# Kernel tuning notes

Measured on AMD Instinct MI355X. Metric: run time of the kernel, lower is better.

Reference implementation:

```python
import jax, jax.numpy as jnp
import numpy as np

C = 256
N_HEAD = 4
GROUPS = 32
EPS = 1e-5
B, H, W = 2, 64, 64


def group_norm(x, gamma, beta):
    # x: [B, C, H, W]; GroupNorm over (C//G, H, W) within each group
    b, c, h, w = x.shape
    xr = x.reshape(b, GROUPS, c // GROUPS, h, w)
    m = xr.mean(axis=(2, 3, 4), keepdims=True)
    v = xr.var(axis=(2, 3, 4), keepdims=True)
    xn = ((xr - m) * jax.lax.rsqrt(v + EPS)).reshape(b, c, h, w)
    return xn * gamma[None, :, None, None] + beta[None, :, None, None]


def setup_inputs() -> dict:
    key = jax.random.key(0)
    ks = jax.random.split(key, 5)
    s = 1.0 / np.sqrt(C)  # fan-in init scale for 1x1 convs
    return {
        "input": jax.random.normal(ks[0], (B, C, H, W), jnp.float32),
        "c": jax.random.normal(ks[1], (B, C, H, W), jnp.float32),
        "gn_w": jnp.ones((C,), jnp.float32),
        "gn_b": jnp.zeros((C,), jnp.float32),
        "wq": jax.random.normal(ks[2], (C, C), jnp.float32) * s,
        "wkv": jax.random.normal(ks[3], (2 * C, C), jnp.float32) * s,
        "wout_w": jax.random.normal(ks[4], (C, C), jnp.float32) * s,
        "wout_b": jnp.zeros((C,), jnp.float32),
    }


def reference(input, c, gn_w, gn_b, wq, wkv, wout_w, wout_b):
    b, ch, h, w = input.shape
    hd = ch // N_HEAD
    n = h * w
    # shared GroupNorm applied to both query source and context
    nq = group_norm(input, gn_w, gn_b)
    nkv = group_norm(c, gn_w, gn_b)
    # 1x1 convs == channel matmuls
    q = jnp.einsum('oc,bchw->bohw', wq, nq).reshape(b, N_HEAD, hd, n)
    kv = jnp.einsum('oc,bchw->bohw', wkv, nkv).reshape(b, N_HEAD, 2 * hd, n)
    k, v = jnp.split(kv, 2, axis=2)  # each [b, nh, hd, n]
    # NOTE: scale is 1/sqrt(channel), as in the source (not 1/sqrt(head_dim))
    attn = jnp.einsum('bncq,bnck->bnqk', q, k) / jnp.sqrt(jnp.float32(ch))
    attn = jax.nn.softmax(attn, axis=-1)
    o = jnp.einsum('bnqk,bnck->bncq', attn, v).reshape(b, ch, h, w)
    o = jnp.einsum('oc,bchw->bohw', wout_w, o) + wout_b[None, :, None, None]
    return o + input
```

## Files before the change

### kernel.cpp

```cpp
#include <hip/hip_runtime.h>


typedef __attribute__((ext_vector_type(8))) short short8;
typedef __attribute__((ext_vector_type(4))) short s4;
typedef __attribute__((ext_vector_type(4))) float f32x4;
typedef __attribute__((ext_vector_type(2))) unsigned int uint2v;

#if __has_builtin(__builtin_amdgcn_exp2f)
#define EXP2(x) __builtin_amdgcn_exp2f(x)
#else
#define EXP2(x) exp2f(x)
#endif

__device__ __forceinline__ unsigned short f2bf(float x) {
    unsigned int u = __builtin_bit_cast(unsigned int, x);
    u += 0x7FFFu + ((u >> 16) & 1u);
    return (unsigned short)(u >> 16);
}

__device__ __forceinline__ unsigned int pk2(float a, float b) {
    unsigned int ua = __builtin_bit_cast(unsigned int, a) + 0x8000u;
    unsigned int ub = __builtin_bit_cast(unsigned int, b) + 0x8000u;
    return (ua >> 16) | (ub & 0xFFFF0000u);
}

__device__ __forceinline__ short8 ld8(const unsigned short* p) {
    return *reinterpret_cast<const short8*>(p);
}

#define MFMA(a, b, c) __builtin_amdgcn_mfma_f32_16x16x32_bf16((a), (b), (c), 0, 0, 0)
#define MFMA16(a, b, c) __builtin_amdgcn_mfma_f32_16x16x16bf16_1k((a), (b), (c), 0, 0, 0)

__global__ __launch_bounds__(256) void gn_stats(const float* __restrict__ x0,
                                                const float* __restrict__ x1,
                                                float* __restrict__ statw) {
    int blk = blockIdx.x;
    int combo = blk >> 2, chunk = blk & 3;
    const float* x = (combo & 64) ? x1 : x0;
    int b = (combo >> 5) & 1, g = combo & 31;
    const float4* base = (const float4*)(x + (size_t)(b * 256 + g * 8) * 4096) + chunk * 2048;
    int tid = threadIdx.x, lane = tid & 63, w = tid >> 6;
    float s = 0.f, s2 = 0.f;
    for (int i = tid; i < 2048; i += 256) {
        float4 v = base[i];
        s  += v.x + v.y + v.z + v.w;
        s2 += v.x * v.x + v.y * v.y + v.z * v.z + v.w * v.w;
    }
    #pragma unroll
    for (int off = 32; off; off >>= 1) {
        s  += __shfl_down(s, off);
        s2 += __shfl_down(s2, off);
    }
    __shared__ float red[8];
    if (lane == 0) { red[w] = s; red[4 + w] = s2; }
    __syncthreads();
    if (tid == 0) {
        float* o = statw + (size_t)(combo * 4 + chunk) * 2;
        o[0] = red[0] + red[1] + red[2] + red[3];
        o[1] = red[4] + red[5] + red[6] + red[7];
    }
}

__global__ __launch_bounds__(256) void gn_norm(const float* __restrict__ x0,
                                               const float* __restrict__ x1,
                                               unsigned short* __restrict__ d0,
                                               unsigned short* __restrict__ d1,
                                               const float* __restrict__ statw,
                                               const float* __restrict__ gamma,
                                               const float* __restrict__ beta) {
    __shared__ unsigned short Xl[64 * 272];
    __shared__ float aL[256], bL[256];
    int blk = blockIdx.x;
    int t = blk >> 7, b = (blk >> 6) & 1, n0 = (blk & 63) * 64;
    const float* x = t ? x1 : x0;
    unsigned short* dst = t ? d1 : d0;
    int tid = threadIdx.x;
    {
        int c = tid, g = c >> 3;
        int combo = (t << 6) | (b << 5) | g;
        const float* sw = statw + (size_t)combo * 8;
        float S  = (sw[0] + sw[2]) + (sw[4] + sw[6]);
        float S2 = (sw[1] + sw[3]) + (sw[5] + sw[7]);
        float mean = S * (1.f / 32768.f);
        float var = S2 * (1.f / 32768.f) - mean * mean;
        float inv = rsqrtf(var + 1e-5f);
        float gm = gamma[c];
        aL[c] = gm * inv;
        bL[c] = beta[c] - mean * gm * inv;
    }
    __syncthreads();
    const float* xb = x + (size_t)b * 256 * 4096 + n0;
    #pragma unroll
    for (int it = 0; it < 16; it++) {
        int c = it * 16 + (tid >> 4);
        int n4 = tid & 15;
        float4 v = *(const float4*)(xb + (size_t)c * 4096 + n4 * 4);
        float a = aL[c], c0 = bL[c];
        int cs = c ^ ((n4 & 7) << 3);
        Xl[(n4 * 4 + 0) * 272 + cs] = f2bf(v.x * a + c0);
        Xl[(n4 * 4 + 1) * 272 + cs] = f2bf(v.y * a + c0);
        Xl[(n4 * 4 + 2) * 272 + cs] = f2bf(v.z * a + c0);
        Xl[(n4 * 4 + 3) * 272 + cs] = f2bf(v.w * a + c0);
    }
    __syncthreads();
    int n = tid >> 2, co = (tid & 3) * 64;
    int key = ((n >> 2) & 7) << 3;
    unsigned short* drow = dst + (size_t)(b * 4096 + n0 + n) * 256 + co;
    #pragma unroll
    for (int j = 0; j < 8; j++) {
        int src = n * 272 + ((co + j * 8) ^ key);
        *(uint4*)(drow + j * 8) = *(const uint4*)&Xl[src];
    }
}

__global__ __launch_bounds__(256) void proj_all(const unsigned short* __restrict__ nqT,
                                                const unsigned short* __restrict__ nkvT,
                                                const float* __restrict__ Wq,
                                                const float* __restrict__ Wkv,
                                                unsigned short* __restrict__ QT,
                                                unsigned short* __restrict__ KF,
                                                unsigned short* __restrict__ VF) {
    __shared__ unsigned short Wl[64 * 264];
    int bb = blockIdx.z;
    int y = blockIdx.y;
    bool isQ = (y < 4);
    int n0 = blockIdx.x * 128;
    int o0 = (isQ ? y : (y - 4)) * 64;
    int tid = threadIdx.x;
    int w = tid >> 6, lane = tid & 63;
    int m16 = lane & 15, g = lane >> 4;

    {
        const float* Wsrc = (isQ ? Wq : Wkv) + (size_t)o0 * 256;
        int row = tid >> 2, c4 = (tid & 3) * 16;
        const float4* wr = (const float4*)(Wsrc + (size_t)row * 256) + c4;
        #pragma unroll
        for (int j = 0; j < 16; j++) {
            float4 v = wr[j];
            unsigned short o4[4] = {f2bf(v.x), f2bf(v.y), f2bf(v.z), f2bf(v.w)};
            *(uint2*)&Wl[row * 264 + (c4 + j) * 4] = *(const uint2*)o4;
        }
    }
    __syncthreads();

    const unsigned short* Xb = (isQ ? nqT : nkvT) + (size_t)bb * 4096 * 256;
    f32x4 acc[2][4] = {};
    int rowA = n0 + w * 32 + m16;
    #pragma unroll
    for (int k0 = 0; k0 < 256; k0 += 32) {
        short8 a0 = ld8(Xb + (size_t)rowA * 256 + k0 + g * 8);
        short8 a1 = ld8(Xb + (size_t)(rowA + 16) * 256 + k0 + g * 8);
        #pragma unroll
        for (int ct = 0; ct < 4; ct++) {
            short8 bf = ld8(&Wl[(ct * 16 + m16) * 264 + k0 + g * 8]);
            acc[0][ct] = MFMA(a0, bf, acc[0][ct]);
            acc[1][ct] = MFMA(a1, bf, acc[1][ct]);
        }
    }
    __syncthreads();

    if (isQ) {
        const float qs = 0.09016844005556021f;
        #pragma unroll
        for (int mt = 0; mt < 2; mt++)
            #pragma unroll
            for (int ct = 0; ct < 4; ct++)
                #pragma unroll
                for (int r = 0; r < 4; r++) {
                    int nl = w * 32 + mt * 16 + g * 4 + r;
                    int ol = ct * 16 + m16;
                    Wl[nl * 68 + ol] = f2bf(acc[mt][ct][r] * qs);
                }
        __syncthreads();
        unsigned short* Ob = QT + (size_t)bb * 4096 * 256;
        int row = tid >> 1, part = tid & 1;
        const unsigned short* src = &Wl[row * 68 + part * 32];
        unsigned short* dstp = Ob + (size_t)(n0 + row) * 256 + o0 + part * 32;
        *(uint4*)(dstp)     = *(const uint4*)(src);
        *(uint4*)(dstp + 8) = *(const uint4*)(src + 8);
        *(uint4*)(dstp + 16) = *(const uint4*)(src + 16);
        *(uint4*)(dstp + 24) = *(const uint4*)(src + 24);
    } else {
        int h2 = o0 >> 7, isV = (o0 >> 6) & 1;
        int bh = bb * 4 + h2;
        #pragma unroll
        for (int mt = 0; mt < 2; mt++)
            #pragma unroll
            for (int ct = 0; ct < 4; ct++)
                #pragma unroll
                for (int r = 0; r < 4; r++) {
                    unsigned short v = f2bf(acc[mt][ct][r]);
                    int off;
                    if (isV) {
                        off = ((w * 4 + ct) * 64 + (m16 + 16 * g)) * 8 + (r + mt * 4);
                    } else {
                        int pos = (g * 4 + r) + 16 * (((ct & 1) << 1) | (m16 >> 3));
                        off = (((w * 2 + mt) * 2 + (ct >> 1)) * 64 + pos) * 8 + (m16 & 7);
                    }
                    Wl[off] = v;
                }
        __syncthreads();
        unsigned short* dstb = (isV ? VF : KF) + (size_t)bh * 262144 + (size_t)n0 * 64;
        #pragma unroll
        for (int j = 0; j < 4; j++) {
            int idx = tid + j * 256;
            *(uint4*)(dstb + idx * 8) = *(const uint4*)&Wl[idx * 8];
        }
    }
}

__global__ __launch_bounds__(512, 2) void attn(const unsigned short* __restrict__ QT,
                                               const unsigned short* __restrict__ KF,
                                               const unsigned short* __restrict__ VF,
                                               unsigned short* __restrict__ OT) {
    __shared__ unsigned short sm[32768];
    int bh = blockIdx.x & 7;
    int qb = blockIdx.x >> 3;
    int bb = bh >> 2, h = bh & 3;
    int tid = threadIdx.x;
    int w = tid >> 6, lane = tid & 63;
    int wq = w & 3, hh = w >> 2;
    int m16 = lane & 15, g = lane >> 4;
    int tloc = tid & 255;

    const unsigned short* KFb = KF + (size_t)bh * 262144;
    const unsigned short* VFb = VF + (size_t)bh * 262144;
    const unsigned short* Qb = QT + (size_t)bb * 4096 * 256;

    int q0 = qb * 64 + wq * 16;
    short8 bq0 = ld8(Qb + (size_t)(q0 + m16) * 256 + h * 64 + g * 8);
    short8 bq1 = ld8(Qb + (size_t)(q0 + m16) * 256 + h * 64 + 32 + g * 8);

    f32x4 acc[4] = {};
    float l = 0.f;

    {
        const uint4* ks = (const uint4*)(KFb + (size_t)(hh * 128) * 1024) + tloc;
        const uint4* vs = (const uint4*)(VFb + (size_t)(hh * 64) * 2048) + tloc;
        uint4 k0 = ks[0], k1 = ks[256], v0 = vs[0], v1 = vs[256];
        uint4* kd = (uint4*)(sm + (hh * 2) * 4096) + tloc;
        uint4* vd = (uint4*)(sm + 16384 + (hh * 2) * 4096) + tloc;
        kd[0] = k0; kd[256] = k1; vd[0] = v0; vd[256] = v1;
    }
    __syncthreads();

    for (int it = 0; it < 32; ++it) {
        int p = it & 1;
        bool pf = (it + 1 < 32);
        uint4 kp0, kp1, vp0, vp1;
        if (pf) {
            const uint4* ks = (const uint4*)(KFb + (size_t)(hh * 128 + (it + 1) * 4) * 1024) + tloc;
            const uint4* vs = (const uint4*)(VFb + (size_t)(hh * 64 + (it + 1) * 2) * 2048) + tloc;
            kp0 = ks[0]; kp1 = ks[256]; vp0 = vs[0]; vp1 = vs[256];
        }

        const unsigned short* Kbuf = sm + (hh * 2 + p) * 4096;
        const unsigned short* Vbuf = sm + 16384 + (hh * 2 + p) * 4096;

        s4 pb[4];
        #pragma unroll
        for (int t16 = 0; t16 < 4; t16++) {
            short8 a0 = ld8(Kbuf + (t16 * 2 + 0) * 512 + lane * 8);
            short8 a1 = ld8(Kbuf + (t16 * 2 + 1) * 512 + lane * 8);
            f32x4 st = {};
            st = MFMA(a0, bq0, st);
            st = MFMA(a1, bq1, st);
            #pragma unroll
            for (int r = 0; r < 4; r++) st[r] = EXP2(st[r]);
            l += (st[0] + st[1]) + (st[2] + st[3]);
            uint2v wv; wv.x = pk2(st[0], st[1]); wv.y = pk2(st[2], st[3]);
            pb[t16] = __builtin_bit_cast(s4, wv);
        }
        #pragma unroll
        for (int T32 = 0; T32 < 2; T32++)
            #pragma unroll
            for (int dt = 0; dt < 4; dt++) {
                short8 va = ld8(Vbuf + (T32 * 4 + dt) * 512 + lane * 8);
                s4 va0 = __builtin_shufflevector(va, va, 0, 1, 2, 3);
                s4 va1 = __builtin_shufflevector(va, va, 4, 5, 6, 7);
                acc[dt] = MFMA16(va0, pb[T32 * 2], acc[dt]);
                acc[dt] = MFMA16(va1, pb[T32 * 2 + 1], acc[dt]);
            }

        if (pf) {
            uint4* kd = (uint4*)(sm + (hh * 2 + (p ^ 1)) * 4096) + tloc;
            uint4* vd = (uint4*)(sm + 16384 + (hh * 2 + (p ^ 1)) * 4096) + tloc;
            kd[0] = kp0; kd[256] = kp1; vd[0] = vp0; vd[256] = vp1;
        }
        __syncthreads();
    }

    l += __shfl_xor(l, 16);
    l += __shfl_xor(l, 32);

    float* Cf = (float*)sm;
    float* Lf = (float*)sm + 4096;
    if (hh == 1) {
        #pragma unroll
        for (int dt = 0; dt < 4; dt++)
            #pragma unroll
            for (int r = 0; r < 4; r++)
                Cf[wq * 1024 + (dt * 16 + g * 4 + r) * 16 + m16] = acc[dt][r];
        if (lane < 16) Lf[wq * 16 + m16] = l;
    }
    __syncthreads();
    if (hh == 0) {
        #pragma unroll
        for (int dt = 0; dt < 4; dt++)
            #pragma unroll
            for (int r = 0; r < 4; r++)
                acc[dt][r] += Cf[wq * 1024 + (dt * 16 + g * 4 + r) * 16 + m16];
        float invl = 1.f / (l + Lf[wq * 16 + m16]);
        unsigned short* Ob = OT + (size_t)bb * 4096 * 256;
        size_t obase = (size_t)(q0 + m16) * 256 + h * 64 + g * 4;
        #pragma unroll
        for (int dt = 0; dt < 4; dt++) {
            unsigned short o4[4];
            #pragma unroll
            for (int r = 0; r < 4; r++) o4[r] = f2bf(acc[dt][r] * invl);
            *(uint2*)&Ob[obase + dt * 16] = *(const uint2*)o4;
        }
    }
}

__global__ __launch_bounds__(256) void outproj(const unsigned short* __restrict__ Ot,
                                               const float* __restrict__ Wo,
                                               const float* __restrict__ bias,
                                               const float* __restrict__ resid,
                                               float* __restrict__ out) {
    __shared__ unsigned short Wl[64 * 264];
    int bb = blockIdx.z;
    int n0 = blockIdx.x * 64;
    int o0 = blockIdx.y * 64;
    int tid = threadIdx.x;
    int w = tid >> 6, lane = tid & 63;
    int m16 = lane & 15, g = lane >> 4;

    {
        const float* Wsrc = Wo + (size_t)o0 * 256;
        int row = tid >> 2, c4 = (tid & 3) * 16;
        const float4* wr = (const float4*)(Wsrc + (size_t)row * 256) + c4;
        #pragma unroll
        for (int j = 0; j < 16; j++) {
            float4 v = wr[j];
            unsigned short o4[4] = {f2bf(v.x), f2bf(v.y), f2bf(v.z), f2bf(v.w)};
            *(uint2*)&Wl[row * 264 + (c4 + j) * 4] = *(const uint2*)o4;
        }
    }
    __syncthreads();

    const unsigned short* Ob = Ot + (size_t)bb * 4096 * 256;
    f32x4 acc[4] = {};
    #pragma unroll
    for (int k0 = 0; k0 < 256; k0 += 32) {
        short8 a = ld8(&Wl[(w * 16 + m16) * 264 + k0 + g * 8]);
        #pragma unroll
        for (int ct = 0; ct < 4; ct++) {
            short8 bf = ld8(Ob + (size_t)(n0 + ct * 16 + m16) * 256 + k0 + g * 8);
            acc[ct] = MFMA(a, bf, acc[ct]);
        }
    }
    float biasr[4];
    #pragma unroll
    for (int r = 0; r < 4; r++) biasr[r] = bias[o0 + w * 16 + g * 4 + r];
    #pragma unroll
    for (int ct = 0; ct < 4; ct++)
        #pragma unroll
        for (int r = 0; r < 4; r++) {
            int o = o0 + w * 16 + g * 4 + r;
            int n = n0 + ct * 16 + m16;
            size_t idx = ((size_t)bb * 256 + o) * 4096 + n;
            out[idx] = acc[ct][r] + biasr[r] + resid[idx];
        }
}

extern "C" void kernel_launch(void* const* d_in, const int* in_sizes, int n_in,
                              void* d_out, int out_size, void* d_ws, size_t ws_size,
                              hipStream_t stream) {
    const float* input  = (const float*)d_in[0];
    const float* cctx   = (const float*)d_in[1];
    const float* gn_w   = (const float*)d_in[2];
    const float* gn_b   = (const float*)d_in[3];
    const float* wq     = (const float*)d_in[4];
    const float* wkv    = (const float*)d_in[5];
    const float* wout_w = (const float*)d_in[6];
    const float* wout_b = (const float*)d_in[7];
    float* out = (float*)d_out;

    unsigned short* ws = (unsigned short*)d_ws;
    unsigned short* nqT  = ws;
    unsigned short* nkvT = nqT + 2097152;
    unsigned short* QT   = nkvT + 2097152;
    unsigned short* KF   = QT + 2097152;
    unsigned short* VF   = KF + 2097152;
    unsigned short* OtT  = VF + 2097152;
    float* statw = (float*)(OtT + 2097152);

    gn_stats<<<512, 256, 0, stream>>>(input, cctx, statw);
    gn_norm<<<256, 256, 0, stream>>>(input, cctx, nqT, nkvT, statw, gn_w, gn_b);
    proj_all<<<dim3(32, 12, 2), 256, 0, stream>>>(nqT, nkvT, wq, wkv, QT, KF, VF);
    attn<<<512, 512, 0, stream>>>(QT, KF, VF, OtT);
    outproj<<<dim3(64, 4, 2), 256, 0, stream>>>(OtT, wout_w, wout_b, input, out);
}
```

Measured before the change: 167.0 us.

## Process two query tiles per wave in attention to reuse K/V fragments

The attention kernel drops from 512 to 256 threads per block. Each wave now computes two 16-row query tiles (32 queries), so every K and V fragment read from LDS feeds twice as many MFMAs. Each thread now stages four uint4 loads per K and V buffer instead of two, and the cross-half reduction handles both query tiles. The aim is to cut LDS traffic and instruction overhead per MFMA. The cost is fewer waves per CU and higher register pressure, which weakens latency hiding.

```diff
diff --git a/kernel.cpp b/kernel.cpp
--- a/kernel.cpp
+++ b/kernel.cpp
@@ -160,7 +160,7 @@
     __syncthreads();
 
     if (isQ) {
-        const float qs = 0.09016844005556021f;
+        const float qscale = 0.09016844005556021f;
         #pragma unroll
         for (int mt = 0; mt < 2; mt++)
             #pragma unroll
@@ -169,7 +169,7 @@
                 for (int r = 0; r < 4; r++) {
                     int nl = w * 32 + mt * 16 + g * 4 + r;
                     int ol = ct * 16 + m16;
-                    Wl[nl * 68 + ol] = f2bf(acc[mt][ct][r] * qs);
+                    Wl[nl * 68 + ol] = f2bf(acc[mt][ct][r] * qscale);
                 }
         __syncthreads();
         unsigned short* Ob = QT + (size_t)bb * 4096 * 256;
@@ -209,7 +209,7 @@
     }
 }
 
-__global__ __launch_bounds__(512, 2) void attn(const unsigned short* __restrict__ QT,
+__global__ __launch_bounds__(256, 2) void attn(const unsigned short* __restrict__ QT,
                                                const unsigned short* __restrict__ KF,
                                                const unsigned short* __restrict__ VF,
                                                unsigned short* __restrict__ OT) {
@@ -219,57 +219,72 @@
     int bb = bh >> 2, h = bh & 3;
     int tid = threadIdx.x;
     int w = tid >> 6, lane = tid & 63;
-    int wq = w & 3, hh = w >> 2;
+    int qs = w & 1, hh = w >> 1;
     int m16 = lane & 15, g = lane >> 4;
-    int tloc = tid & 255;
 
     const unsigned short* KFb = KF + (size_t)bh * 262144;
     const unsigned short* VFb = VF + (size_t)bh * 262144;
     const unsigned short* Qb = QT + (size_t)bb * 4096 * 256;
 
-    int q0 = qb * 64 + wq * 16;
-    short8 bq0 = ld8(Qb + (size_t)(q0 + m16) * 256 + h * 64 + g * 8);
-    short8 bq1 = ld8(Qb + (size_t)(q0 + m16) * 256 + h * 64 + 32 + g * 8);
-
-    f32x4 acc[4] = {};
-    float l = 0.f;
+    int q0 = qb * 64 + qs * 32;
+    short8 bq0A = ld8(Qb + (size_t)(q0 + m16) * 256 + h * 64 + g * 8);
+    short8 bq1A = ld8(Qb + (size_t)(q0 + m16) * 256 + h * 64 + 32 + g * 8);
+    short8 bq0B = ld8(Qb + (size_t)(q0 + 16 + m16) * 256 + h * 64 + g * 8);
+    short8 bq1B = ld8(Qb + (size_t)(q0 + 16 + m16) * 256 + h * 64 + 32 + g * 8);
+
+    f32x4 accA[4] = {}, accB[4] = {};
+    float lA = 0.f, lB = 0.f;
+
+    int sh = tid >> 7;
+    int st = tid & 127;
+
+    const uint4* Kg = (const uint4*)KFb;
+    const uint4* Vg = (const uint4*)VFb;
 
     {
-        const uint4* ks = (const uint4*)(KFb + (size_t)(hh * 128) * 1024) + tloc;
-        const uint4* vs = (const uint4*)(VFb + (size_t)(hh * 64) * 2048) + tloc;
-        uint4 k0 = ks[0], k1 = ks[256], v0 = vs[0], v1 = vs[256];
-        uint4* kd = (uint4*)(sm + (hh * 2) * 4096) + tloc;
-        uint4* vd = (uint4*)(sm + 16384 + (hh * 2) * 4096) + tloc;
-        kd[0] = k0; kd[256] = k1; vd[0] = v0; vd[256] = v1;
+        const uint4* ks = Kg + (size_t)(sh * 32) * 512 + st;
+        const uint4* vs = Vg + (size_t)(sh * 32) * 512 + st;
+        uint4* kd = (uint4*)sm + (sh * 2) * 512 + st;
+        uint4* vd = (uint4*)sm + 2048 + (sh * 2) * 512 + st;
+        #pragma unroll
+        for (int j = 0; j < 4; j++) kd[j * 128] = ks[j * 128];
+        #pragma unroll
+        for (int j = 0; j < 4; j++) vd[j * 128] = vs[j * 128];
     }
     __syncthreads();
 
     for (int it = 0; it < 32; ++it) {
         int p = it & 1;
         bool pf = (it + 1 < 32);
-        uint4 kp0, kp1, vp0, vp1;
+        uint4 kp[4], vp[4];
         if (pf) {
-            const uint4* ks = (const uint4*)(KFb + (size_t)(hh * 128 + (it + 1) * 4) * 1024) + tloc;
-            const uint4* vs = (const uint4*)(VFb + (size_t)(hh * 64 + (it + 1) * 2) * 2048) + tloc;
-            kp0 = ks[0]; kp1 = ks[256]; vp0 = vs[0]; vp1 = vs[256];
+            const uint4* ks = Kg + (size_t)(sh * 32 + it + 1) * 512 + st;
+            const uint4* vs = Vg + (size_t)(sh * 32 + it + 1) * 512 + st;
+            #pragma unroll
+            for (int j = 0; j < 4; j++) kp[j] = ks[j * 128];
+            #pragma unroll
+            for (int j = 0; j < 4; j++) vp[j] = vs[j * 128];
         }
 
         const unsigned short* Kbuf = sm + (hh * 2 + p) * 4096;
         const unsigned short* Vbuf = sm + 16384 + (hh * 2 + p) * 4096;
 
-        s4 pb[4];
+        s4 pbA[4], pbB[4];
         #pragma unroll
         for (int t16 = 0; t16 < 4; t16++) {
             short8 a0 = ld8(Kbuf + (t16 * 2 + 0) * 512 + lane * 8);
             short8 a1 = ld8(Kbuf + (t16 * 2 + 1) * 512 + lane * 8);
-            f32x4 st = {};
-            st = MFMA(a0, bq0, st);
-            st = MFMA(a1, bq1, st);
-            #pragma unroll
-            for (int r = 0; r < 4; r++) st[r] = EXP2(st[r]);
-            l += (st[0] + st[1]) + (st[2] + st[3]);
-            uint2v wv; wv.x = pk2(st[0], st[1]); wv.y = pk2(st[2], st[3]);
-            pb[t16] = __builtin_bit_cast(s4, wv);
+            f32x4 sA = {}, sB = {};
+            sA = MFMA(a0, bq0A, sA); sA = MFMA(a1, bq1A, sA);
+            sB = MFMA(a0, bq0B, sB); sB = MFMA(a1, bq1B, sB);
+            #pragma unroll
+            for (int r = 0; r < 4; r++) { sA[r] = EXP2(sA[r]); sB[r] = EXP2(sB[r]); }
+            lA += (sA[0] + sA[1]) + (sA[2] + sA[3]);
+            lB += (sB[0] + sB[1]) + (sB[2] + sB[3]);
+            uint2v wA; wA.x = pk2(sA[0], sA[1]); wA.y = pk2(sA[2], sA[3]);
+            uint2v wB; wB.x = pk2(sB[0], sB[1]); wB.y = pk2(sB[2], sB[3]);
+            pbA[t16] = __builtin_bit_cast(s4, wA);
+            pbB[t16] = __builtin_bit_cast(s4, wB);
         }
         #pragma unroll
         for (int T32 = 0; T32 < 2; T32++)
@@ -278,20 +293,25 @@
                 short8 va = ld8(Vbuf + (T32 * 4 + dt) * 512 + lane * 8);
                 s4 va0 = __builtin_shufflevector(va, va, 0, 1, 2, 3);
                 s4 va1 = __builtin_shufflevector(va, va, 4, 5, 6, 7);
-                acc[dt] = MFMA16(va0, pb[T32 * 2], acc[dt]);
-                acc[dt] = MFMA16(va1, pb[T32 * 2 + 1], acc[dt]);
+                accA[dt] = MFMA16(va0, pbA[T32 * 2], accA[dt]);
+                accA[dt] = MFMA16(va1, pbA[T32 * 2 + 1], accA[dt]);
+                accB[dt] = MFMA16(va0, pbB[T32 * 2], accB[dt]);
+                accB[dt] = MFMA16(va1, pbB[T32 * 2 + 1], accB[dt]);
             }
 
         if (pf) {
-            uint4* kd = (uint4*)(sm + (hh * 2 + (p ^ 1)) * 4096) + tloc;
-            uint4* vd = (uint4*)(sm + 16384 + (hh * 2 + (p ^ 1)) * 4096) + tloc;
-            kd[0] = kp0; kd[256] = kp1; vd[0] = vp0; vd[256] = vp1;
+            uint4* kd = (uint4*)sm + (sh * 2 + (p ^ 1)) * 512 + st;
+            uint4* vd = (uint4*)sm + 2048 + (sh * 2 + (p ^ 1)) * 512 + st;
+            #pragma unroll
+            for (int j = 0; j < 4; j++) kd[j * 128] = kp[j];
+            #pragma unroll
+            for (int j = 0; j < 4; j++) vd[j * 128] = vp[j];
         }
         __syncthreads();
     }
 
-    l += __shfl_xor(l, 16);
-    l += __shfl_xor(l, 32);
+    lA += __shfl_xor(lA, 16); lA += __shfl_xor(lA, 32);
+    lB += __shfl_xor(lB, 16); lB += __shfl_xor(lB, 32);
 
     float* Cf = (float*)sm;
     float* Lf = (float*)sm + 4096;
@@ -299,26 +319,40 @@
         #pragma unroll
         for (int dt = 0; dt < 4; dt++)
             #pragma unroll
-            for (int r = 0; r < 4; r++)
-                Cf[wq * 1024 + (dt * 16 + g * 4 + r) * 16 + m16] = acc[dt][r];
-        if (lane < 16) Lf[wq * 16 + m16] = l;
+            for (int r = 0; r < 4; r++) {
+                int d = dt * 16 + g * 4 + r;
+                Cf[((qs * 2 + 0) * 64 + d) * 16 + m16] = accA[dt][r];
+                Cf[((qs * 2 + 1) * 64 + d) * 16 + m16] = accB[dt][r];
+            }
+        if (lane < 16) {
+            Lf[(qs * 2 + 0) * 16 + m16] = lA;
+            Lf[(qs * 2 + 1) * 16 + m16] = lB;
+        }
     }
     __syncthreads();
     if (hh == 0) {
         #pragma unroll
         for (int dt = 0; dt < 4; dt++)
             #pragma unroll
-            for (int r = 0; r < 4; r++)
-                acc[dt][r] += Cf[wq * 1024 + (dt * 16 + g * 4 + r) * 16 + m16];
-        float invl = 1.f / (l + Lf[wq * 16 + m16]);
+            for (int r = 0; r < 4; r++) {
+                int d = dt * 16 + g * 4 + r;
+                accA[dt][r] += Cf[((qs * 2 + 0) * 64 + d) * 16 + m16];
+                accB[dt][r] += Cf[((qs * 2 + 1) * 64 + d) * 16 + m16];
+            }
+        float invlA = 1.f / (lA + Lf[(qs * 2 + 0) * 16 + m16]);
+        float invlB = 1.f / (lB + Lf[(qs * 2 + 1) * 16 + m16]);
         unsigned short* Ob = OT + (size_t)bb * 4096 * 256;
-        size_t obase = (size_t)(q0 + m16) * 256 + h * 64 + g * 4;
+        size_t obA = (size_t)(q0 + m16) * 256 + h * 64 + g * 4;
+        size_t obB = (size_t)(q0 + 16 + m16) * 256 + h * 64 + g * 4;
         #pragma unroll
         for (int dt = 0; dt < 4; dt++) {
             unsigned short o4[4];
             #pragma unroll
-            for (int r = 0; r < 4; r++) o4[r] = f2bf(acc[dt][r] * invl);
-            *(uint2*)&Ob[obase + dt * 16] = *(const uint2*)o4;
+            for (int r = 0; r < 4; r++) o4[r] = f2bf(accA[dt][r] * invlA);
+            *(uint2*)&Ob[obA + dt * 16] = *(const uint2*)o4;
+            #pragma unroll
+            for (int r = 0; r < 4; r++) o4[r] = f2bf(accB[dt][r] * invlB);
+            *(uint2*)&Ob[obB + dt * 16] = *(const uint2*)o4;
         }
     }
 }
@@ -399,6 +433,6 @@
     gn_stats<<<512, 256, 0, stream>>>(input, cctx, statw);
     gn_norm<<<256, 256, 0, stream>>>(input, cctx, nqT, nkvT, statw, gn_w, gn_b);
     proj_all<<<dim3(32, 12, 2), 256, 0, stream>>>(nqT, nkvT, wq, wkv, QT, KF, VF);
-    attn<<<512, 512, 0, stream>>>(QT, KF, VF, OtT);
+    attn<<<512, 256, 0, stream>>>(QT, KF, VF, OtT);
     outproj<<<dim3(64, 4, 2), 256, 0, stream>>>(OtT, wout_w, wout_b, input, out);
 }
```

After: 163.4 us. 2.2% less time.
